# Kernel tuning notes

Hardware: AMD Instinct MI355X
Metric: run time of the kernel (lower is better)

The kernel has to match this reference:

```python
import jax, jax.numpy as jnp
import numpy as np
import math

D, NH, DFF = 1024, 16, 4096
B, S = 2, 2048
EPS = 1e-5


def _mha(q_in, k_in, v_in, wq, bq, wk, bk, wv, bv, wo, bo, mask):
    Bq, Sq, Dm = q_in.shape
    Sk = k_in.shape[1]
    dh = Dm // NH
    q = (q_in @ wq + bq).reshape(Bq, Sq, NH, dh).transpose(0, 2, 1, 3)
    k = (k_in @ wk + bk).reshape(Bq, Sk, NH, dh).transpose(0, 2, 1, 3)
    v = (v_in @ wv + bv).reshape(Bq, Sk, NH, dh).transpose(0, 2, 1, 3)
    scores = jnp.einsum('bhqd,bhkd->bhqk', q, k) / math.sqrt(dh)
    scores = jnp.where(mask == 0, jnp.float32(-1e9), scores)
    w = jax.nn.softmax(scores, axis=-1)
    out = jnp.einsum('bhqk,bhkd->bhqd', w, v)
    out = out.transpose(0, 2, 1, 3).reshape(Bq, Sq, Dm)
    return out @ wo + bo


def _ln(x, g, b):
    mu = jnp.mean(x, axis=-1, keepdims=True)
    var = jnp.var(x, axis=-1, keepdims=True)
    return (x - mu) * jax.lax.rsqrt(var + EPS) * g + b


def setup_inputs() -> dict:
    key = jax.random.key(0)
    ks = jax.random.split(key, 20)
    sc = 1.0 / math.sqrt(D)
    inp = {
        'x': jax.random.normal(ks[0], (B, S, D), jnp.float32),
        'encoder_output': jax.random.normal(ks[1], (B, S, D), jnp.float32),
        'src_mask': jnp.ones((B, 1, 1, S), jnp.int32),
        'tgt_mask': jnp.tril(jnp.ones((S, S), jnp.int32))[None, None],
    }
    names = ['s_wq', 's_wk', 's_wv', 's_wo', 'c_wq', 'c_wk', 'c_wv', 'c_wo']
    for i, n in enumerate(names):
        inp[n] = jax.random.normal(ks[2 + i], (D, D), jnp.float32) * sc
        inp[n.replace('w', 'b')] = jnp.zeros((D,), jnp.float32)
    inp['ff_w1'] = jax.random.normal(ks[10], (D, DFF), jnp.float32) * sc
    inp['ff_b1'] = jnp.zeros((DFF,), jnp.float32)
    inp['ff_w2'] = jax.random.normal(ks[11], (DFF, D), jnp.float32) / math.sqrt(DFF)
    inp['ff_b2'] = jnp.zeros((D,), jnp.float32)
    for i in (1, 2, 3):
        inp[f'ln{i}_g'] = jnp.ones((D,), jnp.float32)
        inp[f'ln{i}_b'] = jnp.zeros((D,), jnp.float32)
    return inp


def reference(x, encoder_output, src_mask, tgt_mask,
              s_wq, s_bq, s_wk, s_bk, s_wv, s_bv, s_wo, s_bo,
              c_wq, c_bq, c_wk, c_bk, c_wv, c_bv, c_wo, c_bo,
              ff_w1, ff_b1, ff_w2, ff_b2,
              ln1_g, ln1_b, ln2_g, ln2_b, ln3_g, ln3_b):
    # self-attention + residual + LN (dropout is identity in eval)
    a = _mha(x, x, x, s_wq, s_bq, s_wk, s_bk, s_wv, s_bv, s_wo, s_bo, tgt_mask)
    x = _ln(x + a, ln1_g, ln1_b)
    # cross-attention
    a = _mha(x, encoder_output, encoder_output,
             c_wq, c_bq, c_wk, c_bk, c_wv, c_bv, c_wo, c_bo, src_mask)
    x = _ln(x + a, ln2_g, ln2_b)
    # FFN
    f = jax.nn.relu(x @ ff_w1 + ff_b1) @ ff_w2 + ff_b2
    return _ln(x + f, ln3_g, ln3_b)
```

## Files before the change

kernel.cpp:

```cpp
#include <hip/hip_runtime.h>
#include <hip/hip_bf16.h>
#include <stdint.h>


#define DEV static __device__ __forceinline__

typedef short bf16s;
typedef __attribute__((ext_vector_type(8))) short bf16x8;
typedef __attribute__((ext_vector_type(4))) float f32x4;

DEV short f2b(float f) {
    union { __hip_bfloat16 h; short s; } u;
    u.h = __float2bfloat16(f);
    return u.s;
}

DEV unsigned pk2(float lo, float hi) {
    union { __hip_bfloat162 h; unsigned u; } u;
    u.h = __float22bfloat162_rn(float2{lo, hi});
    return u.u;
}

DEV f32x4 mfma16(bf16x8 a, bf16x8 b, f32x4 c) {
    return __builtin_amdgcn_mfma_f32_16x16x32_bf16(a, b, c, 0, 0, 0);
}

DEV void gload_lds16(const bf16s* g, short* l) {
    __builtin_amdgcn_global_load_lds(
        (const __attribute__((address_space(1))) void*)g,
        (__attribute__((address_space(3))) void*)l,
        16, 0, 0);
}

__global__ __launch_bounds__(256) void cast2_f32_bf16_kernel(
    const float* __restrict__ a, const float* __restrict__ b,
    bf16s* __restrict__ out, int n)
{
    int i = (blockIdx.x * 256 + threadIdx.x) * 8;
    const float* src = (i < n) ? a : b;
    int j = (i < n) ? i : i - n;
    const float4 u = *(const float4*)(src + j);
    const float4 v = *(const float4*)(src + j + 4);
    bf16x8 r;
    r[0] = f2b(u.x); r[1] = f2b(u.y); r[2] = f2b(u.z); r[3] = f2b(u.w);
    r[4] = f2b(v.x); r[5] = f2b(v.y); r[6] = f2b(v.z); r[7] = f2b(v.w);
    *(bf16x8*)(out + i) = r;
}

struct P8 { const float* p[8]; };

__global__ __launch_bounds__(256) void transpose_cast8_kernel(
    P8 srcs, bf16s* __restrict__ dst)
{
    __shared__ short tile[64][65];
    const float* W = srcs.p[blockIdx.z];
    bf16s* Wt = dst + (size_t)blockIdx.z * 1024 * 1024;
    const int n0 = blockIdx.x * 64, k0 = blockIdx.y * 64;
    const int t = threadIdx.x;
#pragma unroll
    for (int it = 0; it < 16; ++it) {
        int idx = it * 256 + t;
        int r = idx >> 6, c = idx & 63;
        tile[r][c] = f2b(W[(size_t)(k0 + r) * 1024 + n0 + c]);
    }
    __syncthreads();
#pragma unroll
    for (int it = 0; it < 16; ++it) {
        int idx = it * 256 + t;
        int r = idx >> 6, c = idx & 63;
        Wt[(size_t)(n0 + r) * 1024 + k0 + c] = tile[c][r];
    }
}

__global__ __launch_bounds__(256) void transpose_cast_kernel(
    const float* __restrict__ W, bf16s* __restrict__ Wt, int Krows, int Ncols)
{
    __shared__ short tile[64][65];
    const int n0 = blockIdx.x * 64, k0 = blockIdx.y * 64;
    const int t = threadIdx.x;
#pragma unroll
    for (int it = 0; it < 16; ++it) {
        int idx = it * 256 + t;
        int r = idx >> 6, c = idx & 63;
        tile[r][c] = f2b(W[(size_t)(k0 + r) * Ncols + n0 + c]);
    }
    __syncthreads();
#pragma unroll
    for (int it = 0; it < 16; ++it) {
        int idx = it * 256 + t;
        int r = idx >> 6, c = idx & 63;
        Wt[(size_t)(n0 + r) * Krows + k0 + c] = tile[c][r];
    }
}

__global__ __launch_bounds__(256) void transpose_v_kernel(
    const bf16s* __restrict__ V, int ldv, bf16s* __restrict__ Vt, int Sk)
{
    __shared__ short tile[64][65];
    const int s0 = blockIdx.x * 64;
    const int bh = blockIdx.y, b = bh >> 4, h = bh & 15;
    const int t = threadIdx.x;
#pragma unroll
    for (int it = 0; it < 16; ++it) {
        int idx = it * 256 + t;
        int r = idx >> 6, c = idx & 63;
        tile[r][c] = V[(size_t)(b * Sk + s0 + r) * ldv + h * 64 + c];
    }
    __syncthreads();
#pragma unroll
    for (int it = 0; it < 16; ++it) {
        int idx = it * 256 + t;
        int r = idx >> 6, c = idx & 63;
        Vt[((size_t)bh * 64 + r) * Sk + s0 + c] = tile[c][r];
    }
}

__global__ void concat3_kernel(const float* a, const float* b, const float* c,
                               float* o, int n)
{
    int i = blockIdx.x * 256 + threadIdx.x;
    if (i < n) { o[i] = a[i]; o[n + i] = b[i]; o[2 * n + i] = c[i]; }
}
__global__ void concat2_kernel(const float* a, const float* b, float* o, int n)
{
    int i = blockIdx.x * 256 + threadIdx.x;
    if (i < n) { o[i] = a[i]; o[n + i] = b[i]; }
}

template<int BM, int BK, int OUT_BF16, int RELU>
__global__ __launch_bounds__(256, (BM == 64 ? 4 : 2))
void gemm_bt_kernel(const bf16s* __restrict__ A, const bf16s* __restrict__ Bt,
                    const float* __restrict__ bias, void* __restrict__ Cp,
                    int M, int N, int K)
{
    constexpr int BN = 128;
    constexpr int WR = BM / 64;
    constexpr int WC = 4 / WR;
    constexpr int TN = BN / WC;
    constexpr int NF = TN / 16;
    constexpr int NSUB = BK / 32;
    constexpr int RA = BM / 64;
    constexpr int ASUB = BM * 32;
    constexpr int BSUB = BN * 32;
    constexpr int ASZ = NSUB * ASUB;
    constexpr int BSZ = NSUB * BSUB;

    __shared__ short As[2 * ASZ];
    __shared__ short Bs[2 * BSZ];

    const int t = threadIdx.x, lane = t & 63, wave = t >> 6;
    const int g = lane >> 4, ln16 = lane & 15;
    const int wr = wave / WC, wc = wave % WC;
    const int rowA0 = blockIdx.y * BM, rowB0 = blockIdx.x * BN;

    const bf16s* Ab = A + (size_t)rowA0 * K;
    const bf16s* Bb = Bt + (size_t)rowB0 * K;

    f32x4 acc[4][NF] = {};

    auto stage = [&](int buf, int k0) {
        short* Ad = As + buf * ASZ;
        short* Bd = Bs + buf * BSZ;
#pragma unroll
        for (int s = 0; s < NSUB; ++s) {
#pragma unroll
            for (int rnd = 0; rnd < RA; ++rnd) {
                int p = rnd * 256 + t;
                int sr = p >> 3, c3 = (p & 7) ^ (sr & 7);
                int r = sr * 2 + (c3 >> 2), c = c3 & 3;
                gload_lds16(Ab + (size_t)r * K + k0 + s * 32 + c * 8,
                            Ad + s * ASUB + (rnd * 256 + wave * 64) * 8);
            }
#pragma unroll
            for (int rnd = 0; rnd < 2; ++rnd) {
                int p = rnd * 256 + t;
                int sr = p >> 3, c3 = (p & 7) ^ (sr & 7);
                int r = sr * 2 + (c3 >> 2), c = c3 & 3;
                gload_lds16(Bb + (size_t)r * K + k0 + s * 32 + c * 8,
                            Bd + s * BSUB + (rnd * 256 + wave * 64) * 8);
            }
        }
    };

    stage(0, 0);
    __syncthreads();
    int cur = 0;
    for (int k0 = 0; k0 < K; k0 += BK) {
        if (k0 + BK < K) stage(cur ^ 1, k0 + BK);
        const short* Ar0 = As + cur * ASZ;
        const short* Br0 = Bs + cur * BSZ;
#pragma unroll
        for (int s = 0; s < NSUB; ++s) {
            const short* Ar = Ar0 + s * ASUB;
            const short* Br = Br0 + s * BSUB;
            bf16x8 af[4], bfr[NF];
#pragma unroll
            for (int m = 0; m < 4; ++m) {
                int r = wr * 64 + m * 16 + ln16;
                int sr = r >> 1, c3 = (r & 1) * 4 + g;
                af[m] = *(const bf16x8*)(Ar + sr * 64 + ((c3 ^ (sr & 7)) * 8));
            }
#pragma unroll
            for (int n = 0; n < NF; ++n) {
                int r = wc * TN + n * 16 + ln16;
                int sr = r >> 1, c3 = (r & 1) * 4 + g;
                bfr[n] = *(const bf16x8*)(Br + sr * 64 + ((c3 ^ (sr & 7)) * 8));
            }
#pragma unroll
            for (int m = 0; m < 4; ++m)
#pragma unroll
                for (int n = 0; n < NF; ++n)
                    acc[m][n] = mfma16(af[m], bfr[n], acc[m][n]);
        }
        __syncthreads();
        cur ^= 1;
    }

    const int row0 = rowA0 + wr * 64, col0 = rowB0 + wc * TN;
#pragma unroll
    for (int n = 0; n < NF; ++n) {
        const int col = col0 + n * 16 + ln16;
        const float bv = bias[col];
#pragma unroll
        for (int m = 0; m < 4; ++m) {
#pragma unroll
            for (int r = 0; r < 4; ++r) {
                int row = row0 + m * 16 + g * 4 + r;
                float v = acc[m][n][r] + bv;
                if (RELU) v = fmaxf(v, 0.f);
                if (OUT_BF16) ((bf16s*)Cp)[(size_t)row * N + col] = f2b(v);
                else          ((float*)Cp)[(size_t)row * N + col] = v;
            }
        }
    }
}

template<int CAUSAL>
__global__ __launch_bounds__(256, 4)
void flash_kernel(const bf16s* __restrict__ Q, int ldq,
                  const bf16s* __restrict__ K, int ldk,
                  const bf16s* __restrict__ Vt,
                  bf16s* __restrict__ O, int ldo,
                  int Sq, int Sk, float scale)
{
    __shared__ short Ks[2 * 64 * 64];
    __shared__ short Vs[2 * 64 * 64];
    __shared__ short Ps[4 * 16 * 64];
    const int t = threadIdx.x, lane = t & 63, wave = t >> 6;
    const int g = lane >> 4, ln16 = lane & 15;

    const int nqt = Sq >> 6;
    const int id = blockIdx.x;
    const int perx = gridDim.x >> 3;
    const int bhPerX = perx / nqt;
    const int idx = id >> 3;
    const int bh = (id & 7) * bhPerX + idx / nqt;
    const int j = idx % nqt;
    const int qt = CAUSAL ? ((j & 1) ? (j >> 1) : (nqt - 1 - (j >> 1))) : j;
    const int b = bh >> 4, h = bh & 15;
    const int q0 = qt * 64;
    const float sc2 = scale * 1.44269504f;
    const float thrRaw = 8.0f / sc2;

    bf16x8 aq[2];
    {
        const size_t qrow = (size_t)(b * Sq + q0 + wave * 16 + ln16);
#pragma unroll
        for (int kk = 0; kk < 2; ++kk)
            aq[kk] = *(const bf16x8*)(Q + qrow * ldq + h * 64 + kk * 32 + g * 8);
    }

    int qvOff[2][4];
    int paOff[2];
    int pWr[4];
#pragma unroll
    for (int kk = 0; kk < 2; ++kk) {
        paOff[kk] = ln16 * 64 + (((kk * 4 + g) ^ (ln16 & 7)) * 8);
#pragma unroll
        for (int n = 0; n < 4; ++n) {
            int key = n * 16 + ln16;
            qvOff[kk][n] = key * 64 + (((kk * 4 + g) ^ (key & 7)) * 8);
        }
    }
#pragma unroll
    for (int n = 0; n < 4; ++n) {
        int c = n * 2 + (g >> 1);
        pWr[n] = ln16 * 64 + ((c ^ (ln16 & 7)) * 8) +
                 (((g & 1) ^ (ln16 >> 3)) * 4);
    }
    const int x0 = (ln16 >> 3) * 4;

    int sgOffK[2], sgOffV[2], sgLds[2];
#pragma unroll
    for (int rnd = 0; rnd < 2; ++rnd) {
        int p = rnd * 256 + t;
        int r = p >> 3, c = (p & 7) ^ (r & 7);
        sgOffK[rnd] = r * ldk + c * 8;
        sgOffV[rnd] = r * Sk + c * 8;
        sgLds[rnd]  = (rnd * 256 + wave * 64) * 8;
    }

    float m_raw = -1e30f, l_sum = 0.f;
    f32x4 oa[4] = {};

    const int nkt = CAUSAL ? (qt + 1) : (Sk >> 6);
    const bf16s* kcur = K + (size_t)b * Sk * ldk + h * 64;
    const bf16s* vcur = Vt + (size_t)bh * 64 * Sk;
    short* myP = Ps + wave * 1024;

    auto stage = [&](int buf) {
        short* Kd = Ks + (buf << 12);
        short* Vd = Vs + (buf << 12);
#pragma unroll
        for (int rnd = 0; rnd < 2; ++rnd)
            gload_lds16(kcur + sgOffK[rnd], Kd + sgLds[rnd]);
#pragma unroll
        for (int rnd = 0; rnd < 2; ++rnd)
            gload_lds16(vcur + sgOffV[rnd], Vd + sgLds[rnd]);
    };

    stage(0);
    kcur += (size_t)64 * ldk; vcur += 64;
    __syncthreads();
    int cur = 0;

    for (int kt = 0; kt < nkt; ++kt) {
        if (kt + 1 < nkt) {
            stage(cur ^ 1);
            kcur += (size_t)64 * ldk; vcur += 64;
        }
        const short* Kr = Ks + (cur << 12);
        const short* Vr = Vs + (cur << 12);

        f32x4 sa[4] = {};
        __builtin_amdgcn_s_setprio(1);
#pragma unroll
        for (int kk = 0; kk < 2; ++kk)
#pragma unroll
            for (int n = 0; n < 4; ++n)
                sa[n] = mfma16(*(const bf16x8*)(Kr + qvOff[kk][n]), aq[kk], sa[n]);
        __builtin_amdgcn_s_setprio(0);

        float sv[4][4];
        const bool diag = CAUSAL && (kt == qt);
#pragma unroll
        for (int n = 0; n < 4; ++n)
#pragma unroll
            for (int r = 0; r < 4; ++r) {
                float s = sa[n][r];
                if (diag && (n * 16 + g * 4 + r > wave * 16 + ln16)) s = -1e30f;
                sv[n][r] = s;
            }

        float rm = fmaxf(fmaxf(sv[0][0], sv[0][1]), sv[0][2]);
        rm = fmaxf(fmaxf(rm, sv[0][3]), sv[1][0]);
        rm = fmaxf(fmaxf(rm, sv[1][1]), sv[1][2]);
        rm = fmaxf(fmaxf(rm, sv[1][3]), sv[2][0]);
        rm = fmaxf(fmaxf(rm, sv[2][1]), sv[2][2]);
        rm = fmaxf(fmaxf(rm, sv[2][3]), sv[3][0]);
        rm = fmaxf(fmaxf(rm, sv[3][1]), sv[3][2]);
        rm = fmaxf(rm, sv[3][3]);
        rm = fmaxf(rm, __shfl_xor(rm, 16, 64));
        rm = fmaxf(rm, __shfl_xor(rm, 32, 64));

        if (!__all(rm <= m_raw + thrRaw)) {
            const float mnew = fmaxf(m_raw, rm);
            const float al = __builtin_amdgcn_exp2f((m_raw - mnew) * sc2);
            m_raw = mnew;
            l_sum *= al;
            float alr[4];
#pragma unroll
            for (int r = 0; r < 4; ++r)
                alr[r] = __shfl(al, g * 4 + r, 64);
#pragma unroll
            for (int n = 0; n < 4; ++n)
#pragma unroll
                for (int r = 0; r < 4; ++r)
                    oa[n][r] *= alr[r];
        }
        const float nm = -m_raw * sc2;

        float rs = 0.f;
#pragma unroll
        for (int n = 0; n < 4; ++n)
#pragma unroll
            for (int r = 0; r < 4; ++r) {
                float p = __builtin_amdgcn_exp2f(fmaf(sv[n][r], sc2, nm));
                sv[n][r] = p;
                rs += p;
            }
        rs += __shfl_xor(rs, 16, 64);
        rs += __shfl_xor(rs, 32, 64);
        l_sum += rs;

#pragma unroll
        for (int n = 0; n < 4; ++n) {
            uint2 w;
            w.x = pk2(sv[n][0], sv[n][1]);
            w.y = pk2(sv[n][2], sv[n][3]);
            *(uint2*)(myP + pWr[n]) = w;
        }
        asm volatile("s_waitcnt lgkmcnt(0)" ::: "memory");

        __builtin_amdgcn_s_setprio(1);
#pragma unroll
        for (int kk = 0; kk < 2; ++kk) {
            union { bf16x8 v; uint2 u2[2]; } pu;
            pu.u2[0] = *(const uint2*)(myP + paOff[kk] + x0);
            pu.u2[1] = *(const uint2*)(myP + paOff[kk] + (x0 ^ 4));
            bf16x8 pa = pu.v;
#pragma unroll
            for (int n = 0; n < 4; ++n)
                oa[n] = mfma16(pa, *(const bf16x8*)(Vr + qvOff[kk][n]), oa[n]);
        }
        __builtin_amdgcn_s_setprio(0);
        __syncthreads();
        cur ^= 1;
    }

    const float inv = 1.f / l_sum;
    float invr[4];
#pragma unroll
    for (int r = 0; r < 4; ++r)
        invr[r] = __shfl(inv, g * 4 + r, 64);
#pragma unroll
    for (int n = 0; n < 4; ++n)
#pragma unroll
        for (int r = 0; r < 4; ++r) {
            int q = q0 + wave * 16 + g * 4 + r;
            int d = h * 64 + n * 16 + ln16;
            O[(size_t)(b * Sq + q) * ldo + d] = f2b(oa[n][r] * invr[r]);
        }
}

template<int WRITE_BF16>
__global__ __launch_bounds__(256)
void add_ln_kernel(const float* __restrict__ X, const float* __restrict__ A,
                   const float* __restrict__ G, const float* __restrict__ Bb,
                   float* __restrict__ Y, bf16s* __restrict__ Yb)
{
    const int row = blockIdx.x, t = threadIdx.x;
    const int lane = t & 63, w = t >> 6;
    const size_t base = (size_t)row * 1024 + t * 4;
    const float4 xv = *(const float4*)(X + base);
    const float4 av = *(const float4*)(A + base);
    float4 v;
    v.x = xv.x + av.x; v.y = xv.y + av.y; v.z = xv.z + av.z; v.w = xv.w + av.w;
    float s = v.x + v.y + v.z + v.w;
    float q = v.x * v.x + v.y * v.y + v.z * v.z + v.w * v.w;
#pragma unroll
    for (int x = 1; x < 64; x <<= 1) {
        s += __shfl_xor(s, x, 64);
        q += __shfl_xor(q, x, 64);
    }
    __shared__ float red[8];
    if (lane == 0) { red[w] = s; red[4 + w] = q; }
    __syncthreads();
    s = red[0] + red[1] + red[2] + red[3];
    q = red[4] + red[5] + red[6] + red[7];
    const float mu = s * (1.f / 1024.f);
    const float var = q * (1.f / 1024.f) - mu * mu;
    const float rstd = rsqrtf(var + 1e-5f);
    const float4 gv = *(const float4*)(G + t * 4);
    const float4 bv = *(const float4*)(Bb + t * 4);
    float o0 = (v.x - mu) * rstd * gv.x + bv.x;
    float o1 = (v.y - mu) * rstd * gv.y + bv.y;
    float o2 = (v.z - mu) * rstd * gv.z + bv.z;
    float o3 = (v.w - mu) * rstd * gv.w + bv.w;
    float4 ov; ov.x = o0; ov.y = o1; ov.z = o2; ov.w = o3;
    *(float4*)(Y + base) = ov;
    if (WRITE_BF16) {
        short4 yb;
        yb.x = f2b(o0); yb.y = f2b(o1); yb.z = f2b(o2); yb.w = f2b(o3);
        *(short4*)(Yb + base) = yb;
    }
}

extern "C" void kernel_launch(void* const* d_in, const int* in_sizes, int n_in,
                              void* d_out, int out_size, void* d_ws, size_t ws_size,
                              hipStream_t stream)
{
    constexpr int Dm = 1024, DFF = 4096, Bq = 2, S = 2048;
    constexpr int NT = Bq * S;
    constexpr size_t MM = (size_t)Dm * Dm;

    const float* x    = (const float*)d_in[0];
    const float* enc  = (const float*)d_in[1];
    const float* s_wq = (const float*)d_in[4];  const float* s_bq = (const float*)d_in[5];
    const float* s_wk = (const float*)d_in[6];  const float* s_bk = (const float*)d_in[7];
    const float* s_wv = (const float*)d_in[8];  const float* s_bv = (const float*)d_in[9];
    const float* s_wo = (const float*)d_in[10]; const float* s_bo = (const float*)d_in[11];
    const float* c_wq = (const float*)d_in[12]; const float* c_bq = (const float*)d_in[13];
    const float* c_wk = (const float*)d_in[14]; const float* c_bk = (const float*)d_in[15];
    const float* c_wv = (const float*)d_in[16]; const float* c_bv = (const float*)d_in[17];
    const float* c_wo = (const float*)d_in[18]; const float* c_bo = (const float*)d_in[19];
    const float* ffw1 = (const float*)d_in[20]; const float* ffb1 = (const float*)d_in[21];
    const float* ffw2 = (const float*)d_in[22]; const float* ffb2 = (const float*)d_in[23];
    const float* ln1g = (const float*)d_in[24]; const float* ln1b = (const float*)d_in[25];
    const float* ln2g = (const float*)d_in[26]; const float* ln2b = (const float*)d_in[27];
    const float* ln3g = (const float*)d_in[28]; const float* ln3b = (const float*)d_in[29];

    char* ws = (char*)d_ws;
    size_t off = 0;
    auto alloc = [&](size_t bytes) -> char* {
        char* p = ws + off;
        off += (bytes + 255) & ~(size_t)255;
        return p;
    };

    bf16s* xbf   = (bf16s*)alloc((size_t)NT * Dm * 2);
    bf16s* encbf = (bf16s*)alloc((size_t)NT * Dm * 2);
    bf16s* wAll  = (bf16s*)alloc(8 * MM * 2);
    bf16s* w1T   = (bf16s*)alloc((size_t)Dm * DFF * 2);
    bf16s* w2T   = (bf16s*)alloc((size_t)Dm * DFF * 2);
    float* bqkv  = (float*)alloc((size_t)3 * Dm * 4);
    float* bkvc  = (float*)alloc((size_t)2 * Dm * 4);
    bf16s* QKV   = (bf16s*)alloc((size_t)NT * 3 * Dm * 2);
    bf16s* Vt    = (bf16s*)alloc((size_t)NT * Dm * 2);
    bf16s* AO    = (bf16s*)alloc((size_t)NT * Dm * 2);
    float* Pbuf  = (float*)alloc((size_t)NT * Dm * 4);
    float* x1f   = (float*)alloc((size_t)NT * Dm * 4);
    bf16s* x1bf  = (bf16s*)alloc((size_t)NT * Dm * 2);
    float* x2f   = (float*)alloc((size_t)NT * Dm * 4);
    bf16s* x2bf  = (bf16s*)alloc((size_t)NT * Dm * 2);
    bf16s* Hbuf  = (bf16s*)alloc((size_t)NT * DFF * 2);
    (void)ws_size; (void)in_sizes; (void)n_in; (void)out_size;

    bf16s* wqkvT = wAll;
    bf16s* woTs  = wAll + 3 * MM;
    bf16s* wqTc  = wAll + 4 * MM;
    bf16s* wkvTc = wAll + 5 * MM;
    bf16s* woTc  = wAll + 7 * MM;

    cast2_f32_bf16_kernel<<<2 * NT * Dm / 8 / 256, 256, 0, stream>>>(
        x, enc, xbf, NT * Dm);
    P8 srcs = {{s_wq, s_wk, s_wv, s_wo, c_wq, c_wk, c_wv, c_wo}};
    transpose_cast8_kernel<<<dim3(16, 16, 8), 256, 0, stream>>>(srcs, wAll);
    transpose_cast_kernel<<<dim3(64, 16), 256, 0, stream>>>(ffw1, w1T, Dm, DFF);
    transpose_cast_kernel<<<dim3(16, 64), 256, 0, stream>>>(ffw2, w2T, DFF, Dm);
    concat3_kernel<<<4, 256, 0, stream>>>(s_bq, s_bk, s_bv, bqkv, Dm);
    concat2_kernel<<<4, 256, 0, stream>>>(c_bk, c_bv, bkvc, Dm);

    gemm_bt_kernel<128, 64, 1, 0><<<dim3(24, 32), 256, 0, stream>>>(
        xbf, wqkvT, bqkv, QKV, NT, 3 * Dm, Dm);
    transpose_v_kernel<<<dim3(32, 32), 256, 0, stream>>>(
        QKV + 2 * Dm, 3 * Dm, Vt, S);
    flash_kernel<1><<<dim3(1024), 256, 0, stream>>>(
        QKV, 3 * Dm, QKV + Dm, 3 * Dm, Vt, AO, Dm, S, S, 0.125f);
    gemm_bt_kernel<64, 32, 0, 0><<<dim3(8, 64), 256, 0, stream>>>(
        AO, woTs, s_bo, Pbuf, NT, Dm, Dm);
    add_ln_kernel<1><<<NT, 256, 0, stream>>>(x, Pbuf, ln1g, ln1b, x1f, x1bf);

    bf16s* Q2  = QKV;
    bf16s* KV2 = QKV + (size_t)NT * Dm;
    gemm_bt_kernel<64, 32, 1, 0><<<dim3(8, 64), 256, 0, stream>>>(
        x1bf, wqTc, c_bq, Q2, NT, Dm, Dm);
    gemm_bt_kernel<128, 64, 1, 0><<<dim3(16, 32), 256, 0, stream>>>(
        encbf, wkvTc, bkvc, KV2, NT, 2 * Dm, Dm);
    transpose_v_kernel<<<dim3(32, 32), 256, 0, stream>>>(
        KV2 + Dm, 2 * Dm, Vt, S);
    flash_kernel<0><<<dim3(1024), 256, 0, stream>>>(
        Q2, Dm, KV2, 2 * Dm, Vt, AO, Dm, S, S, 0.125f);
    gemm_bt_kernel<64, 32, 0, 0><<<dim3(8, 64), 256, 0, stream>>>(
        AO, woTc, c_bo, Pbuf, NT, Dm, Dm);
    add_ln_kernel<1><<<NT, 256, 0, stream>>>(x1f, Pbuf, ln2g, ln2b, x2f, x2bf);

    gemm_bt_kernel<128, 64, 1, 1><<<dim3(32, 32), 256, 0, stream>>>(
        x2bf, w1T, ffb1, Hbuf, NT, DFF, Dm);
    gemm_bt_kernel<64, 32, 0, 0><<<dim3(8, 64), 256, 0, stream>>>(
        Hbuf, w2T, ffb2, Pbuf, NT, Dm, DFF);
    add_ln_kernel<0><<<NT, 256, 0, stream>>>(
        x2f, Pbuf, ln3g, ln3b, (float*)d_out, nullptr);
}
```

Baseline: 576.9 us.

## Split-K the fp32-output projection GEMMs and reduce partials in add+LayerNorm

The three GEMMs that write fp32 output (the two attention output projections and FFN W2) now split K across blockIdx.z into 2 or 4 slices. Each slice writes its own partial slab into an enlarged Pbuf, and the add+LayerNorm kernel sums the slabs before normalising, with bias added only by slice 0. This raises the block count from 512 to 1024 or 2048, which fills the GPU better for these small-N GEMMs. The cost is extra fp32 partial-slab traffic written and then read back by the LN kernel, plus a larger workspace.

```diff
diff --git a/kernel.cpp b/kernel.cpp
--- a/kernel.cpp
+++ b/kernel.cpp
@@ -127,7 +127,7 @@
     if (i < n) { o[i] = a[i]; o[n + i] = b[i]; }
 }
 
-template<int BM, int BK, int OUT_BF16, int RELU>
+template<int BM, int BK, int OUT_BF16, int RELU, int NSPLIT>
 __global__ __launch_bounds__(256, (BM == 64 ? 4 : 2))
 void gemm_bt_kernel(const bf16s* __restrict__ A, const bf16s* __restrict__ Bt,
                     const float* __restrict__ bias, void* __restrict__ Cp,
@@ -152,9 +152,11 @@
     const int g = lane >> 4, ln16 = lane & 15;
     const int wr = wave / WC, wc = wave % WC;
     const int rowA0 = blockIdx.y * BM, rowB0 = blockIdx.x * BN;
-
-    const bf16s* Ab = A + (size_t)rowA0 * K;
-    const bf16s* Bb = Bt + (size_t)rowB0 * K;
+    const int z = (NSPLIT > 1) ? (int)blockIdx.z : 0;
+    const int kLen = K / NSPLIT;
+
+    const bf16s* Ab = A + (size_t)rowA0 * K + (size_t)z * kLen;
+    const bf16s* Bb = Bt + (size_t)rowB0 * K + (size_t)z * kLen;
 
     f32x4 acc[4][NF] = {};
 
@@ -185,8 +187,8 @@
     stage(0, 0);
     __syncthreads();
     int cur = 0;
-    for (int k0 = 0; k0 < K; k0 += BK) {
-        if (k0 + BK < K) stage(cur ^ 1, k0 + BK);
+    for (int k0 = 0; k0 < kLen; k0 += BK) {
+        if (k0 + BK < kLen) stage(cur ^ 1, k0 + BK);
         const short* Ar0 = As + cur * ASZ;
         const short* Br0 = Bs + cur * BSZ;
 #pragma unroll
@@ -217,10 +219,11 @@
     }
 
     const int row0 = rowA0 + wr * 64, col0 = rowB0 + wc * TN;
+    float* Cz = (float*)Cp + (size_t)z * M * N;
 #pragma unroll
     for (int n = 0; n < NF; ++n) {
         const int col = col0 + n * 16 + ln16;
-        const float bv = bias[col];
+        const float bv = (z == 0) ? bias[col] : 0.f;
 #pragma unroll
         for (int m = 0; m < 4; ++m) {
 #pragma unroll
@@ -229,7 +232,7 @@
                 float v = acc[m][n][r] + bv;
                 if (RELU) v = fmaxf(v, 0.f);
                 if (OUT_BF16) ((bf16s*)Cp)[(size_t)row * N + col] = f2b(v);
-                else          ((float*)Cp)[(size_t)row * N + col] = v;
+                else          Cz[(size_t)row * N + col] = v;
             }
         }
     }
@@ -433,19 +436,23 @@
         }
 }
 
-template<int WRITE_BF16>
+template<int WRITE_BF16, int NSUM>
 __global__ __launch_bounds__(256)
 void add_ln_kernel(const float* __restrict__ X, const float* __restrict__ A,
                    const float* __restrict__ G, const float* __restrict__ Bb,
                    float* __restrict__ Y, bf16s* __restrict__ Yb)
 {
+    constexpr size_t SLAB = (size_t)4096 * 1024;
     const int row = blockIdx.x, t = threadIdx.x;
     const int lane = t & 63, w = t >> 6;
     const size_t base = (size_t)row * 1024 + t * 4;
     const float4 xv = *(const float4*)(X + base);
-    const float4 av = *(const float4*)(A + base);
-    float4 v;
-    v.x = xv.x + av.x; v.y = xv.y + av.y; v.z = xv.z + av.z; v.w = xv.w + av.w;
+    float4 v = xv;
+#pragma unroll
+    for (int s = 0; s < NSUM; ++s) {
+        const float4 av = *(const float4*)(A + s * SLAB + base);
+        v.x += av.x; v.y += av.y; v.z += av.z; v.w += av.w;
+    }
     float s = v.x + v.y + v.z + v.w;
     float q = v.x * v.x + v.y * v.y + v.z * v.z + v.w * v.w;
 #pragma unroll
@@ -518,7 +525,7 @@
     bf16s* QKV   = (bf16s*)alloc((size_t)NT * 3 * Dm * 2);
     bf16s* Vt    = (bf16s*)alloc((size_t)NT * Dm * 2);
     bf16s* AO    = (bf16s*)alloc((size_t)NT * Dm * 2);
-    float* Pbuf  = (float*)alloc((size_t)NT * Dm * 4);
+    float* Pbuf  = (float*)alloc((size_t)4 * NT * Dm * 4);
     float* x1f   = (float*)alloc((size_t)NT * Dm * 4);
     bf16s* x1bf  = (bf16s*)alloc((size_t)NT * Dm * 2);
     float* x2f   = (float*)alloc((size_t)NT * Dm * 4);
@@ -541,34 +548,34 @@
     concat3_kernel<<<4, 256, 0, stream>>>(s_bq, s_bk, s_bv, bqkv, Dm);
     concat2_kernel<<<4, 256, 0, stream>>>(c_bk, c_bv, bkvc, Dm);
 
-    gemm_bt_kernel<128, 64, 1, 0><<<dim3(24, 32), 256, 0, stream>>>(
+    gemm_bt_kernel<128, 64, 1, 0, 1><<<dim3(24, 32), 256, 0, stream>>>(
         xbf, wqkvT, bqkv, QKV, NT, 3 * Dm, Dm);
     transpose_v_kernel<<<dim3(32, 32), 256, 0, stream>>>(
         QKV + 2 * Dm, 3 * Dm, Vt, S);
     flash_kernel<1><<<dim3(1024), 256, 0, stream>>>(
         QKV, 3 * Dm, QKV + Dm, 3 * Dm, Vt, AO, Dm, S, S, 0.125f);
-    gemm_bt_kernel<64, 32, 0, 0><<<dim3(8, 64), 256, 0, stream>>>(
+    gemm_bt_kernel<64, 32, 0, 0, 2><<<dim3(8, 64, 2), 256, 0, stream>>>(
         AO, woTs, s_bo, Pbuf, NT, Dm, Dm);
-    add_ln_kernel<1><<<NT, 256, 0, stream>>>(x, Pbuf, ln1g, ln1b, x1f, x1bf);
+    add_ln_kernel<1, 2><<<NT, 256, 0, stream>>>(x, Pbuf, ln1g, ln1b, x1f, x1bf);
 
     bf16s* Q2  = QKV;
     bf16s* KV2 = QKV + (size_t)NT * Dm;
-    gemm_bt_kernel<64, 32, 1, 0><<<dim3(8, 64), 256, 0, stream>>>(
+    gemm_bt_kernel<64, 32, 1, 0, 1><<<dim3(8, 64), 256, 0, stream>>>(
         x1bf, wqTc, c_bq, Q2, NT, Dm, Dm);
-    gemm_bt_kernel<128, 64, 1, 0><<<dim3(16, 32), 256, 0, stream>>>(
+    gemm_bt_kernel<128, 64, 1, 0, 1><<<dim3(16, 32), 256, 0, stream>>>(
         encbf, wkvTc, bkvc, KV2, NT, 2 * Dm, Dm);
     transpose_v_kernel<<<dim3(32, 32), 256, 0, stream>>>(
         KV2 + Dm, 2 * Dm, Vt, S);
     flash_kernel<0><<<dim3(1024), 256, 0, stream>>>(
         Q2, Dm, KV2, 2 * Dm, Vt, AO, Dm, S, S, 0.125f);
-    gemm_bt_kernel<64, 32, 0, 0><<<dim3(8, 64), 256, 0, stream>>>(
+    gemm_bt_kernel<64, 32, 0, 0, 2><<<dim3(8, 64, 2), 256, 0, stream>>>(
         AO, woTc, c_bo, Pbuf, NT, Dm, Dm);
-    add_ln_kernel<1><<<NT, 256, 0, stream>>>(x1f, Pbuf, ln2g, ln2b, x2f, x2bf);
-
-    gemm_bt_kernel<128, 64, 1, 1><<<dim3(32, 32), 256, 0, stream>>>(
+    add_ln_kernel<1, 2><<<NT, 256, 0, stream>>>(x1f, Pbuf, ln2g, ln2b, x2f, x2bf);
+
+    gemm_bt_kernel<128, 64, 1, 1, 1><<<dim3(32, 32), 256, 0, stream>>>(
         x2bf, w1T, ffb1, Hbuf, NT, DFF, Dm);
-    gemm_bt_kernel<64, 32, 0, 0><<<dim3(8, 64), 256, 0, stream>>>(
+    gemm_bt_kernel<64, 32, 0, 0, 4><<<dim3(8, 64, 4), 256, 0, stream>>>(
         Hbuf, w2T, ffb2, Pbuf, NT, Dm, DFF);
-    add_ln_kernel<0><<<NT, 256, 0, stream>>>(
+    add_ln_kernel<0, 4><<<NT, 256, 0, stream>>>(
         x2f, Pbuf, ln3g, ln3b, (float*)d_out, nullptr);
 }
```

Result: slower. 591.6 us (+2.5%).
